# Performance work log

Hardware: AMD Instinct MI355X
Metric: run time of the kernel (lower is better)

The kernel has to match this reference:

```python
import jax, jax.numpy as jnp
import numpy as np
from jax import lax

T = 64
TAU = 2.0
ALPHA = 4.0  # spikingjelly surrogate.Sigmoid default
V_TH = 1.0

@jax.custom_vjp
def spike(v):
    # Heaviside(v) with sigmoid surrogate gradient
    return (v >= 0.0).astype(v.dtype)

def _spike_fwd(v):
    return spike(v), v

def _spike_bwd(v, g):
    s = jax.nn.sigmoid(ALPHA * v)
    return (g * ALPHA * s * (1.0 - s),)

spike.defvjp(_spike_fwd, _spike_bwd)

def setup_inputs() -> dict:
    key = jax.random.key(0)
    k1, k2, k3 = jax.random.split(key, 3)
    x = jax.random.normal(k1, (2048, 28, 28), dtype=jnp.float32)
    W1 = jax.random.normal(k2, (1024, 784), dtype=jnp.float32) * (1.0 / np.sqrt(784))
    W2 = jax.random.normal(k3, (10, 1024), dtype=jnp.float32) * (1.0 / np.sqrt(1024))
    return {"x": x, "W1": W1, "W2": W2}

def _lif_step(v, c):
    # decay_input=True: v += (x - (v - v_reset)) / tau, v_reset = 0
    v = v + (c - v) / TAU
    s = spike(v - V_TH)
    v = v * (1.0 - s)  # hard reset to 0
    return v, s

def reference(x, W1, W2):
    B = x.shape[0]
    xf = x.reshape(B, -1)                      # [B, 784]
    c1 = xf @ W1.T                              # [B, 1024], identical every timestep
    v1_0 = jnp.zeros((B, W1.shape[0]), x.dtype)
    v2_0 = jnp.zeros((B, W2.shape[0]), x.dtype)

    def step(carry, _):
        v1, v2 = carry
        v1, s1 = _lif_step(v1, c1)              # [B, 1024]
        c2 = s1 @ W2.T                          # [B, 10]
        v2, s2 = _lif_step(v2, c2)              # [B, 10]
        return (v1, v2), s2

    _, out = lax.scan(step, (v1_0, v2_0), None, length=T)
    return out  # [T, B, 10]
```

## Files before the change

kernel.cpp:

```cpp
#include <hip/hip_runtime.h>
#include <stdint.h>

typedef unsigned long long u64;
typedef unsigned int u32;

#define T_STEPS 64
#define KDIM 784
#define N1 1024
#define NB 2048
#define N2 10

__global__ void k_w2t(const float* __restrict__ W2, float* __restrict__ W2T) {
    int j = blockIdx.x * blockDim.x + threadIdx.x;
    if (j >= N1) return;
    float r[12];
#pragma unroll
    for (int i = 0; i < 10; ++i) r[i] = W2[i * N1 + j];
    r[10] = 0.f; r[11] = 0.f;
#pragma unroll
    for (int i = 0; i < 12; ++i) W2T[j * 12 + i] = r[i];
}

__global__ __launch_bounds__(256) void k_transpose2(
    const float* __restrict__ X, float* __restrict__ Xt,
    const float* __restrict__ W1, float* __restrict__ W1t)
{
    __shared__ float t[32][33];
    int b = blockIdx.x;
    const float* src; float* dst; int R;
    int tile_r, tile_c;
    if (b < 1600) { src = X;  dst = Xt;  R = NB; tile_r = b / 25; tile_c = b % 25; }
    else { b -= 1600; src = W1; dst = W1t; R = N1; tile_r = b / 25; tile_c = b % 25; }

    const int tx = threadIdx.x & 31, ty = threadIdx.x >> 5;
    const int r0 = tile_r << 5, c0 = tile_c << 5;

#pragma unroll
    for (int i = 0; i < 32; i += 8) {
        int c = c0 + tx;
        t[ty + i][tx] = (c < KDIM) ? src[(size_t)(r0 + ty + i) * KDIM + c] : 0.f;
    }
    __syncthreads();
#pragma unroll
    for (int i = 0; i < 32; i += 8) {
        int c = c0 + ty + i;
        if (c < KDIM) dst[(size_t)c * R + r0 + tx] = t[tx][ty + i];
    }
}

__global__ __launch_bounds__(256) void k_gemm_lif1(
    const float* __restrict__ Xt,
    const float* __restrict__ W1t,
    u64* __restrict__ bits)
{
    const int tid  = threadIdx.x;
    const int wv   = tid >> 6;
    const int lane = tid & 63;
    const int bx   = blockIdx.x;

    const int n0 = (bx & 15) << 6;
    const int m0 = __builtin_amdgcn_readfirstlane(((bx >> 4) << 6) + (wv << 4));

    const int n = n0 + lane;
    const float*  __restrict__ wrow = W1t + n;
    const float4* __restrict__ xrow = (const float4*)(Xt + m0);

    float acc[16];
#pragma unroll
    for (int i = 0; i < 16; ++i) acc[i] = 0.f;

#pragma unroll 4
    for (int k = 0; k < KDIM; ++k) {
        float a  = wrow[(size_t)k * N1];
        float4 x0 = xrow[(size_t)k * 512 + 0];
        float4 x1 = xrow[(size_t)k * 512 + 1];
        float4 x2 = xrow[(size_t)k * 512 + 2];
        float4 x3 = xrow[(size_t)k * 512 + 3];
        acc[ 0] = fmaf(a, x0.x, acc[ 0]); acc[ 1] = fmaf(a, x0.y, acc[ 1]);
        acc[ 2] = fmaf(a, x0.z, acc[ 2]); acc[ 3] = fmaf(a, x0.w, acc[ 3]);
        acc[ 4] = fmaf(a, x1.x, acc[ 4]); acc[ 5] = fmaf(a, x1.y, acc[ 5]);
        acc[ 6] = fmaf(a, x1.z, acc[ 6]); acc[ 7] = fmaf(a, x1.w, acc[ 7]);
        acc[ 8] = fmaf(a, x2.x, acc[ 8]); acc[ 9] = fmaf(a, x2.y, acc[ 9]);
        acc[10] = fmaf(a, x2.z, acc[10]); acc[11] = fmaf(a, x2.w, acc[11]);
        acc[12] = fmaf(a, x3.x, acc[12]); acc[13] = fmaf(a, x3.y, acc[13]);
        acc[14] = fmaf(a, x3.z, acc[14]); acc[15] = fmaf(a, x3.w, acc[15]);
    }

    float v[16];
    u32 blo[16], bhi[16];
#pragma unroll
    for (int u = 0; u < 16; ++u) { v[u] = 0.f; blo[u] = 0u; bhi[u] = 0u; }
    for (int t = 0; t < 32; ++t) {
#pragma unroll
        for (int u = 0; u < 16; ++u) {
            v[u] += (acc[u] - v[u]) * 0.5f;
            bool s = v[u] >= 1.0f;
            blo[u] |= (s ? 1u : 0u) << t;
            v[u] = s ? 0.f : v[u];
        }
    }
    for (int t = 0; t < 32; ++t) {
#pragma unroll
        for (int u = 0; u < 16; ++u) {
            v[u] += (acc[u] - v[u]) * 0.5f;
            bool s = v[u] >= 1.0f;
            bhi[u] |= (s ? 1u : 0u) << t;
            v[u] = s ? 0.f : v[u];
        }
    }

    u64* bp = bits + (size_t)m0 * N1 + n;
#pragma unroll
    for (int u = 0; u < 16; ++u)
        bp[(size_t)u * N1] = ((u64)bhi[u] << 32) | (u64)blo[u];
}

__global__ __launch_bounds__(256) void k_lif2(
    const u64* __restrict__ bits, const float* __restrict__ W2T,
    float* __restrict__ out)
{
    __shared__ u64  masksS[4][N1];
    __shared__ u32  idxS[4][N1];
    __shared__ float c2S[4][64][12];
    __shared__ float s2S[4][64][10];

    const int tid  = threadIdx.x;
    const int w    = tid >> 6;
    const int lane = tid & 63;
    const int b    = (blockIdx.x << 2) + w;

    const u64* row = bits + (size_t)b * N1;

    int nact = 0;
#pragma unroll
    for (int it = 0; it < 16; ++it) {
        u64 m = row[lane + (it << 6)];
        u64 ball = __ballot(m != 0ULL);
        int pos = nact + __popcll(ball & ((1ULL << lane) - 1ULL));
        if (m != 0ULL) { masksS[w][pos] = m; idxS[w][pos] = lane + (it << 6); }
        nact += __popcll(ball);
    }

    float acc[10];
#pragma unroll
    for (int i = 0; i < 10; ++i) acc[i] = 0.f;

#define LIF2_BODY(A)                                                      \
    {                                                                     \
        u64 m = masksS[w][(A)];                                           \
        int j = __builtin_amdgcn_readfirstlane((int)idxS[w][(A)]);        \
        float sf = (float)((m >> lane) & 1ULL);                           \
        const float* wr = W2T + j * 12;                                   \
        float4 w0 = *(const float4*)(wr);                                 \
        float4 w1 = *(const float4*)(wr + 4);                             \
        float2 w2 = *(const float2*)(wr + 8);                             \
        acc[0] += sf * w0.x; acc[1] += sf * w0.y;                         \
        acc[2] += sf * w0.z; acc[3] += sf * w0.w;                         \
        acc[4] += sf * w1.x; acc[5] += sf * w1.y;                         \
        acc[6] += sf * w1.z; acc[7] += sf * w1.w;                         \
        acc[8] += sf * w2.x; acc[9] += sf * w2.y;                         \
    }

    int a = 0;
    for (; a + 2 <= nact; a += 2) { LIF2_BODY(a); LIF2_BODY(a + 1); }
    if (a < nact) LIF2_BODY(a);
#undef LIF2_BODY

#pragma unroll
    for (int i = 0; i < 10; ++i) c2S[w][lane][i] = acc[i];
    __syncthreads();

    if (tid < 40) {
        const int w2 = tid / 10, i = tid % 10;
        float v2 = 0.f;
        for (int t = 0; t < 64; ++t) {
            float cc = c2S[w2][t][i];
            v2 += (cc - v2) * 0.5f;
            bool s = v2 >= 1.0f;
            s2S[w2][t][i] = s ? 1.f : 0.f;
            v2 = s ? 0.f : v2;
        }
    }
    __syncthreads();

    const int b0 = blockIdx.x << 2;
    for (int idx = tid; idx < 64 * 40; idx += 256) {
        int t = idx / 40, r = idx % 40;
        out[(size_t)t * (NB * N2) + (size_t)b0 * N2 + r] = s2S[r / 10][t][r % 10];
    }
}

extern "C" void kernel_launch(void* const* d_in, const int* in_sizes, int n_in,
                              void* d_out, int out_size, void* d_ws, size_t ws_size,
                              hipStream_t stream) {
    const float* X  = (const float*)d_in[0];
    const float* W1 = (const float*)d_in[1];
    const float* W2 = (const float*)d_in[2];
    float* out = (float*)d_out;

    char* ws = (char*)d_ws;
    u64*   bits = (u64*)ws;
    float* W2T  = (float*)(ws + (size_t)NB * N1 * 8);
    float* Xt   = (float*)(ws + (size_t)NB * N1 * 8 + 65536);
    float* W1t  = Xt + (size_t)KDIM * NB;

    k_w2t<<<dim3((N1 + 255) / 256), dim3(256), 0, stream>>>(W2, W2T);
    k_transpose2<<<dim3(2400), dim3(256), 0, stream>>>(X, Xt, W1, W1t);

    k_gemm_lif1<<<dim3(512), dim3(256), 0, stream>>>(Xt, W1t, bits);

    k_lif2<<<dim3(NB / 4), dim3(256), 0, stream>>>(bits, W2T, out);
}
```

Before: 201.9 us.

## Tile GEMM through double-buffered LDS and split LIF2 rows across waves

The first-layer GEMM now stages 16-deep K slices of Xt and W1t into double-buffered shared memory using direct global-to-LDS loads, and computes a 4x4 register tile per thread instead of each lane streaming its own W1 column from global memory. This is meant to raise data reuse and cut global traffic. The second-layer kernel gives each batch row a full block, with each wave scanning a quarter of the hidden units; partial sums are reduced in shared memory before the LIF recurrence. That adds parallelism per row, but the reduction changes summation order and adds a barrier.

After: 164.2 us. 1.23x faster.

```diff
diff --git a/kernel.cpp b/kernel.cpp
--- a/kernel.cpp
+++ b/kernel.cpp
@@ -48,52 +48,86 @@
     }
 }
 
+#define NSTEP (KDIM / 16)
+
+typedef const __attribute__((address_space(1))) void gas_void;
+typedef __attribute__((address_space(3))) void las_void;
+
 __global__ __launch_bounds__(256) void k_gemm_lif1(
     const float* __restrict__ Xt,
     const float* __restrict__ W1t,
     u64* __restrict__ bits)
 {
+    __shared__ __align__(16) float A2[2][16][64];
+    __shared__ __align__(16) float B2[2][16][64];
+
     const int tid  = threadIdx.x;
-    const int wv   = tid >> 6;
     const int lane = tid & 63;
-    const int bx   = blockIdx.x;
-
-    const int n0 = (bx & 15) << 6;
-    const int m0 = __builtin_amdgcn_readfirstlane(((bx >> 4) << 6) + (wv << 4));
-
-    const int n = n0 + lane;
-    const float*  __restrict__ wrow = W1t + n;
-    const float4* __restrict__ xrow = (const float4*)(Xt + m0);
-
-    float acc[16];
-#pragma unroll
-    for (int i = 0; i < 16; ++i) acc[i] = 0.f;
-
-#pragma unroll 4
-    for (int k = 0; k < KDIM; ++k) {
-        float a  = wrow[(size_t)k * N1];
-        float4 x0 = xrow[(size_t)k * 512 + 0];
-        float4 x1 = xrow[(size_t)k * 512 + 1];
-        float4 x2 = xrow[(size_t)k * 512 + 2];
-        float4 x3 = xrow[(size_t)k * 512 + 3];
-        acc[ 0] = fmaf(a, x0.x, acc[ 0]); acc[ 1] = fmaf(a, x0.y, acc[ 1]);
-        acc[ 2] = fmaf(a, x0.z, acc[ 2]); acc[ 3] = fmaf(a, x0.w, acc[ 3]);
-        acc[ 4] = fmaf(a, x1.x, acc[ 4]); acc[ 5] = fmaf(a, x1.y, acc[ 5]);
-        acc[ 6] = fmaf(a, x1.z, acc[ 6]); acc[ 7] = fmaf(a, x1.w, acc[ 7]);
-        acc[ 8] = fmaf(a, x2.x, acc[ 8]); acc[ 9] = fmaf(a, x2.y, acc[ 9]);
-        acc[10] = fmaf(a, x2.z, acc[10]); acc[11] = fmaf(a, x2.w, acc[11]);
-        acc[12] = fmaf(a, x3.x, acc[12]); acc[13] = fmaf(a, x3.y, acc[13]);
-        acc[14] = fmaf(a, x3.z, acc[14]); acc[15] = fmaf(a, x3.w, acc[15]);
-    }
-
-    float v[16];
+    const int tx   = tid & 15;
+    const int ty   = tid >> 4;
+    const int bm   = blockIdx.y << 6;
+    const int bn   = blockIdx.x << 6;
+
+    const int w4   = __builtin_amdgcn_readfirstlane((tid >> 6) << 2);
+    const int srow = w4 + (lane >> 4);
+    const int scol = (lane & 15) << 2;
+
+    const float* gA = Xt  + (size_t)srow * NB + bm + scol;
+    const float* gB = W1t + (size_t)srow * N1 + bn + scol;
+
+#define STAGE(pp, t)                                                          \
+    {                                                                         \
+        __builtin_amdgcn_global_load_lds((gas_void*)(gA + (size_t)(t) * (16 * NB)), \
+                                         (las_void*)&A2[pp][w4][0], 16, 0, 0); \
+        __builtin_amdgcn_global_load_lds((gas_void*)(gB + (size_t)(t) * (16 * N1)), \
+                                         (las_void*)&B2[pp][w4][0], 16, 0, 0); \
+    }
+
+    float acc[4][4];
+#pragma unroll
+    for (int r = 0; r < 4; ++r)
+#pragma unroll
+        for (int c = 0; c < 4; ++c) acc[r][c] = 0.f;
+
+    STAGE(0, 0);
+    asm volatile("s_waitcnt vmcnt(0)" ::: "memory");
+    __builtin_amdgcn_s_barrier();
+    __builtin_amdgcn_sched_barrier(0);
+
+    int p = 0;
+    for (int t = 0; t < NSTEP; ++t) {
+        if (t + 1 < NSTEP) STAGE(p ^ 1, t + 1);
+#pragma unroll
+        for (int kk = 0; kk < 16; ++kk) {
+            float4 av = *(const float4*)(&A2[p][kk][ty << 2]);
+            float4 bv = *(const float4*)(&B2[p][kk][tx << 2]);
+            acc[0][0] = fmaf(av.x, bv.x, acc[0][0]); acc[0][1] = fmaf(av.x, bv.y, acc[0][1]);
+            acc[0][2] = fmaf(av.x, bv.z, acc[0][2]); acc[0][3] = fmaf(av.x, bv.w, acc[0][3]);
+            acc[1][0] = fmaf(av.y, bv.x, acc[1][0]); acc[1][1] = fmaf(av.y, bv.y, acc[1][1]);
+            acc[1][2] = fmaf(av.y, bv.z, acc[1][2]); acc[1][3] = fmaf(av.y, bv.w, acc[1][3]);
+            acc[2][0] = fmaf(av.z, bv.x, acc[2][0]); acc[2][1] = fmaf(av.z, bv.y, acc[2][1]);
+            acc[2][2] = fmaf(av.z, bv.z, acc[2][2]); acc[2][3] = fmaf(av.z, bv.w, acc[2][3]);
+            acc[3][0] = fmaf(av.w, bv.x, acc[3][0]); acc[3][1] = fmaf(av.w, bv.y, acc[3][1]);
+            acc[3][2] = fmaf(av.w, bv.z, acc[3][2]); acc[3][3] = fmaf(av.w, bv.w, acc[3][3]);
+        }
+        asm volatile("s_waitcnt vmcnt(0)" ::: "memory");
+        __builtin_amdgcn_s_barrier();
+        __builtin_amdgcn_sched_barrier(0);
+        p ^= 1;
+    }
+#undef STAGE
+
+    float c[16], v[16];
     u32 blo[16], bhi[16];
 #pragma unroll
-    for (int u = 0; u < 16; ++u) { v[u] = 0.f; blo[u] = 0u; bhi[u] = 0u; }
+    for (int u = 0; u < 16; ++u) {
+        c[u] = acc[u >> 2][u & 3];
+        v[u] = 0.f; blo[u] = 0u; bhi[u] = 0u;
+    }
     for (int t = 0; t < 32; ++t) {
 #pragma unroll
         for (int u = 0; u < 16; ++u) {
-            v[u] += (acc[u] - v[u]) * 0.5f;
+            v[u] += (c[u] - v[u]) * 0.5f;
             bool s = v[u] >= 1.0f;
             blo[u] |= (s ? 1u : 0u) << t;
             v[u] = s ? 0.f : v[u];
@@ -102,42 +136,45 @@
     for (int t = 0; t < 32; ++t) {
 #pragma unroll
         for (int u = 0; u < 16; ++u) {
-            v[u] += (acc[u] - v[u]) * 0.5f;
+            v[u] += (c[u] - v[u]) * 0.5f;
             bool s = v[u] >= 1.0f;
             bhi[u] |= (s ? 1u : 0u) << t;
             v[u] = s ? 0.f : v[u];
         }
     }
-
-    u64* bp = bits + (size_t)m0 * N1 + n;
-#pragma unroll
-    for (int u = 0; u < 16; ++u)
-        bp[(size_t)u * N1] = ((u64)bhi[u] << 32) | (u64)blo[u];
+#pragma unroll
+    for (int u = 0; u < 16; ++u) {
+        int r = u >> 2, cc = u & 3;
+        bits[(size_t)(bm + (ty << 2) + r) * N1 + (bn + (tx << 2) + cc)] =
+            ((u64)bhi[u] << 32) | (u64)blo[u];
+    }
 }
 
 __global__ __launch_bounds__(256) void k_lif2(
     const u64* __restrict__ bits, const float* __restrict__ W2T,
     float* __restrict__ out)
 {
-    __shared__ u64  masksS[4][N1];
-    __shared__ u32  idxS[4][N1];
+    __shared__ u64  masksS[N1];
+    __shared__ u32  idxS[N1];
     __shared__ float c2S[4][64][12];
-    __shared__ float s2S[4][64][10];
+    __shared__ float s2S[64][10];
 
     const int tid  = threadIdx.x;
     const int w    = tid >> 6;
     const int lane = tid & 63;
-    const int b    = (blockIdx.x << 2) + w;
+    const int b    = blockIdx.x;
 
     const u64* row = bits + (size_t)b * N1;
+    const int base_j = w << 8;
 
     int nact = 0;
 #pragma unroll
-    for (int it = 0; it < 16; ++it) {
-        u64 m = row[lane + (it << 6)];
+    for (int it = 0; it < 4; ++it) {
+        int j = base_j + (it << 6) + lane;
+        u64 m = row[j];
         u64 ball = __ballot(m != 0ULL);
         int pos = nact + __popcll(ball & ((1ULL << lane) - 1ULL));
-        if (m != 0ULL) { masksS[w][pos] = m; idxS[w][pos] = lane + (it << 6); }
+        if (m != 0ULL) { masksS[base_j + pos] = m; idxS[base_j + pos] = j; }
         nact += __popcll(ball);
     }
 
@@ -147,8 +184,8 @@
 
 #define LIF2_BODY(A)                                                      \
     {                                                                     \
-        u64 m = masksS[w][(A)];                                           \
-        int j = __builtin_amdgcn_readfirstlane((int)idxS[w][(A)]);        \
+        u64 m = masksS[(A)];                                              \
+        int j = __builtin_amdgcn_readfirstlane((int)idxS[(A)]);           \
         float sf = (float)((m >> lane) & 1ULL);                           \
         const float* wr = W2T + j * 12;                                   \
         float4 w0 = *(const float4*)(wr);                                 \
@@ -162,31 +199,30 @@
     }
 
     int a = 0;
-    for (; a + 2 <= nact; a += 2) { LIF2_BODY(a); LIF2_BODY(a + 1); }
-    if (a < nact) LIF2_BODY(a);
+    for (; a + 2 <= nact; a += 2) { LIF2_BODY(base_j + a); LIF2_BODY(base_j + a + 1); }
+    if (a < nact) LIF2_BODY(base_j + a);
 #undef LIF2_BODY
 
 #pragma unroll
     for (int i = 0; i < 10; ++i) c2S[w][lane][i] = acc[i];
     __syncthreads();
 
-    if (tid < 40) {
-        const int w2 = tid / 10, i = tid % 10;
+    if (tid < 10) {
+        const int i = tid;
         float v2 = 0.f;
         for (int t = 0; t < 64; ++t) {
-            float cc = c2S[w2][t][i];
+            float cc = ((c2S[0][t][i] + c2S[1][t][i]) + c2S[2][t][i]) + c2S[3][t][i];
             v2 += (cc - v2) * 0.5f;
             bool s = v2 >= 1.0f;
-            s2S[w2][t][i] = s ? 1.f : 0.f;
+            s2S[t][i] = s ? 1.f : 0.f;
             v2 = s ? 0.f : v2;
         }
     }
     __syncthreads();
 
-    const int b0 = blockIdx.x << 2;
-    for (int idx = tid; idx < 64 * 40; idx += 256) {
-        int t = idx / 40, r = idx % 40;
-        out[(size_t)t * (NB * N2) + (size_t)b0 * N2 + r] = s2S[r / 10][t][r % 10];
+    for (int idx = tid; idx < 64 * 10; idx += 256) {
+        int t = idx / 10, i = idx % 10;
+        out[(size_t)t * (NB * N2) + (size_t)b * N2 + i] = s2S[t][i];
     }
 }
 
@@ -207,7 +243,8 @@
     k_w2t<<<dim3((N1 + 255) / 256), dim3(256), 0, stream>>>(W2, W2T);
     k_transpose2<<<dim3(2400), dim3(256), 0, stream>>>(X, Xt, W1, W1t);
 
-    k_gemm_lif1<<<dim3(512), dim3(256), 0, stream>>>(Xt, W1t, bits);
-
-    k_lif2<<<dim3(NB / 4), dim3(256), 0, stream>>>(bits, W2T, out);
-}
+    dim3 g1(N1 / 64, NB / 64);
+    k_gemm_lif1<<<g1, dim3(256), 0, stream>>>(Xt, W1t, bits);
+
+    k_lif2<<<dim3(NB), dim3(256), 0, stream>>>(bits, W2T, out);
+}
```
